# Kernel tuning notes

Hardware: AMD Instinct MI355X
Metric: run time of the kernel (lower is better)

Reference implementation:

```python
import jax, jax.numpy as jnp
import numpy as np

N_SECTORS = 10          # = 1.0 / slice_range with normalized slice indices in [0, 1)
SLICE_RANGE = 0.1
PAIRWISE_EPS = 1e-6     # torch.nn.functional.pairwise_distance default eps (added to the diff)


def setup_inputs() -> dict:
    key = jax.random.key(0)
    k1, k2, k3, k4 = jax.random.split(key, 4)
    source_embeddings = jax.random.normal(k1, (200000, 256), dtype=jnp.float32)
    source_sectors = jax.random.randint(k2, (200000,), 0, N_SECTORS, dtype=jnp.int32)
    target_embeddings = jax.random.normal(k3, (100000, 256), dtype=jnp.float32)
    target_slice_idx = jax.random.uniform(k4, (100000,), dtype=jnp.float32)
    return {
        "source_embeddings": source_embeddings,
        "source_sectors": source_sectors,
        "target_embeddings": target_embeddings,
        "target_slice_idx": target_slice_idx,
    }


def reference(source_embeddings, source_sectors, target_embeddings, target_slice_idx):
    # cluster_centers[i] = mean of source_embeddings where source_sectors == i
    sums = jax.ops.segment_sum(source_embeddings, source_sectors, num_segments=N_SECTORS)  # [S, D]
    counts = jax.ops.segment_sum(
        jnp.ones((source_embeddings.shape[0],), dtype=source_embeddings.dtype),
        source_sectors, num_segments=N_SECTORS)                                            # [S]
    cluster_centers = sums / counts[:, None]                                               # [S, D]

    # get_sectors_from_index: bucket normalized slice index into sectors of width slice_range
    target_sectors = jnp.clip(
        jnp.floor(target_slice_idx / SLICE_RANGE).astype(jnp.int32), 0, N_SECTORS - 1)     # [N]

    cc = cluster_centers[target_sectors]                                                   # [N, D] gather

    # F.pairwise_distance with p=2, eps=1e-6: ||x1 - x2 + eps||_2
    diff = target_embeddings - cc + PAIRWISE_EPS
    distances = jnp.sqrt(jnp.sum(diff * diff, axis=-1))                                    # [N]
    return distances.mean()
```

## Files before the change

kernel.cpp:

```cpp
#include <hip/hip_runtime.h>
#include <math.h>

#define D      256
#define NSEC   10
#define EPS    1e-6f
#define SLICE  0.1f

#define WS_SUMS 0
#define WS_CNT  (NSEC * D)
#define WS_DIST (NSEC * D + NSEC)
#define WS_ZERO_FLOATS (NSEC * D + NSEC + 1)

__global__ void k_zero(float* __restrict__ ws) {
    int i = blockIdx.x * blockDim.x + threadIdx.x;
    if (i < WS_ZERO_FLOATS) ws[i] = 0.f;
}

__global__ __launch_bounds__(256) void k_sums(const float* __restrict__ emb,
                                              const int* __restrict__ sec,
                                              float* __restrict__ ws, int nrows) {
    const int lane = threadIdx.x & 63;
    const int wid  = threadIdx.x >> 6;
    const int gw   = blockIdx.x * 4 + wid;
    const int nw   = gridDim.x * 4;

    float4 acc[NSEC];
    float  cnt[NSEC];
#pragma unroll
    for (int s = 0; s < NSEC; ++s) { acc[s] = make_float4(0.f, 0.f, 0.f, 0.f); cnt[s] = 0.f; }

    const float* ep = emb + (size_t)lane * 4;

    auto accum = [&](int sv, float4 v) {
        const int s = __builtin_amdgcn_readfirstlane(sv);
#pragma unroll
        for (int ss = 0; ss < NSEC; ++ss) {
            if (s == ss) {
                acc[ss].x += v.x; acc[ss].y += v.y; acc[ss].z += v.z; acc[ss].w += v.w;
                cnt[ss] += 1.f;
            }
        }
    };

    int r = gw;
    for (; r + 3 * nw < nrows; r += 4 * nw) {
        const int s0 = sec[r];
        const int s1 = sec[r + nw];
        const int s2 = sec[r + 2 * nw];
        const int s3 = sec[r + 3 * nw];
        const float4 v0 = *reinterpret_cast<const float4*>(ep + (size_t)r * D);
        const float4 v1 = *reinterpret_cast<const float4*>(ep + (size_t)(r + nw) * D);
        const float4 v2 = *reinterpret_cast<const float4*>(ep + (size_t)(r + 2 * nw) * D);
        const float4 v3 = *reinterpret_cast<const float4*>(ep + (size_t)(r + 3 * nw) * D);
        accum(s0, v0); accum(s1, v1); accum(s2, v2); accum(s3, v3);
    }
    for (; r < nrows; r += nw)
        accum(sec[r], *reinterpret_cast<const float4*>(ep + (size_t)r * D));

    __shared__ float lsum[NSEC * D];
    __shared__ float lcnt[NSEC];
    for (int i = threadIdx.x; i < NSEC * D; i += 256) lsum[i] = 0.f;
    if (threadIdx.x < NSEC) lcnt[threadIdx.x] = 0.f;
    __syncthreads();

    for (int w = 0; w < 4; ++w) {
        if (wid == w) {
#pragma unroll
            for (int ss = 0; ss < NSEC; ++ss) {
                float* p = &lsum[ss * D + lane * 4];
                p[0] += acc[ss].x; p[1] += acc[ss].y; p[2] += acc[ss].z; p[3] += acc[ss].w;
                if (lane == 0) lcnt[ss] += cnt[ss];
            }
        }
        __syncthreads();
    }

#pragma unroll
    for (int ss = 0; ss < NSEC; ++ss)
        atomicAdd(&ws[WS_SUMS + ss * D + threadIdx.x], lsum[ss * D + threadIdx.x]);
    if (threadIdx.x < NSEC)
        atomicAdd(&ws[WS_CNT + threadIdx.x], lcnt[threadIdx.x]);
}

__global__ __launch_bounds__(256) void k_dist(const float* __restrict__ temb,
                                              const float* __restrict__ tsl,
                                              float* __restrict__ ws, int nrows) {
    __shared__ float lc[NSEC * D];
    for (int i = threadIdx.x; i < NSEC * D; i += 256) {
        const int s = i >> 8;
        lc[i] = ws[WS_SUMS + i] / ws[WS_CNT + s];
    }
    __syncthreads();

    const int lane = threadIdx.x & 63;
    const int wid  = threadIdx.x >> 6;
    const int gw   = blockIdx.x * 4 + wid;
    const int nw   = gridDim.x * 4;

    const float* tp = temb + (size_t)lane * 4;

    auto rowdist = [&](float si, float4 v) -> float {
        int s = (int)floorf(si / SLICE);
        s = s < 0 ? 0 : (s > NSEC - 1 ? NSEC - 1 : s);
        const float4 c = *reinterpret_cast<const float4*>(&lc[s * D + lane * 4]);
        const float dx = v.x - c.x + EPS;
        const float dy = v.y - c.y + EPS;
        const float dz = v.z - c.z + EPS;
        const float dw = v.w - c.w + EPS;
        float loc = dx * dx + dy * dy + dz * dz + dw * dw;
#pragma unroll
        for (int off = 32; off >= 1; off >>= 1) loc += __shfl_xor(loc, off, 64);
        return loc;
    };

    float wacc = 0.f;
    int r = gw;
    for (; r + 3 * nw < nrows; r += 4 * nw) {
        const float t0 = tsl[r];
        const float t1 = tsl[r + nw];
        const float t2 = tsl[r + 2 * nw];
        const float t3 = tsl[r + 3 * nw];
        const float4 v0 = *reinterpret_cast<const float4*>(tp + (size_t)r * D);
        const float4 v1 = *reinterpret_cast<const float4*>(tp + (size_t)(r + nw) * D);
        const float4 v2 = *reinterpret_cast<const float4*>(tp + (size_t)(r + 2 * nw) * D);
        const float4 v3 = *reinterpret_cast<const float4*>(tp + (size_t)(r + 3 * nw) * D);
        float l0 = rowdist(t0, v0);
        float l1 = rowdist(t1, v1);
        float l2 = rowdist(t2, v2);
        float l3 = rowdist(t3, v3);
        if (lane == 0) wacc += sqrtf(l0) + sqrtf(l1) + sqrtf(l2) + sqrtf(l3);
    }
    for (; r < nrows; r += nw) {
        float l = rowdist(tsl[r], *reinterpret_cast<const float4*>(tp + (size_t)r * D));
        if (lane == 0) wacc += sqrtf(l);
    }

    __shared__ float wsum[4];
    if (lane == 0) wsum[wid] = wacc;
    __syncthreads();
    if (threadIdx.x == 0)
        atomicAdd(&ws[WS_DIST], wsum[0] + wsum[1] + wsum[2] + wsum[3]);
}

__global__ void k_final(const float* __restrict__ ws, float* __restrict__ out, float invN) {
    out[0] = ws[WS_DIST] * invN;
}

extern "C" void kernel_launch(void* const* d_in, const int* in_sizes, int n_in,
                              void* d_out, int out_size, void* d_ws, size_t ws_size,
                              hipStream_t stream) {
    const float* semb = (const float*)d_in[0];
    const int*   ssec = (const int*)d_in[1];
    const float* temb = (const float*)d_in[2];
    const float* tsl  = (const float*)d_in[3];
    float* ws  = (float*)d_ws;
    float* out = (float*)d_out;
    const int nS = in_sizes[1];
    const int nT = in_sizes[3];

    hipLaunchKernelGGL(k_zero, dim3((WS_ZERO_FLOATS + 255) / 256), dim3(256), 0, stream, ws);
    hipLaunchKernelGGL(k_sums, dim3(1024), dim3(256), 0, stream, semb, ssec, ws, nS);
    hipLaunchKernelGGL(k_dist, dim3(1024), dim3(256), 0, stream, temb, tsl, ws, nT);
    hipLaunchKernelGGL(k_final, dim3(1), dim3(1), 0, stream, ws, out, 1.0f / (float)nT);
}
```

Measured before the change: 112.9 us.

## Replace global atomics with per-block slabs and a dedicated center-reduction kernel

```diff
diff --git a/kernel.cpp b/kernel.cpp
--- a/kernel.cpp
+++ b/kernel.cpp
@@ -6,19 +6,19 @@
 #define EPS    1e-6f
 #define SLICE  0.1f
 
-#define WS_SUMS 0
-#define WS_CNT  (NSEC * D)
-#define WS_DIST (NSEC * D + NSEC)
-#define WS_ZERO_FLOATS (NSEC * D + NSEC + 1)
-
-__global__ void k_zero(float* __restrict__ ws) {
-    int i = blockIdx.x * blockDim.x + threadIdx.x;
-    if (i < WS_ZERO_FLOATS) ws[i] = 0.f;
-}
-
-__global__ __launch_bounds__(256) void k_sums(const float* __restrict__ emb,
-                                              const int* __restrict__ sec,
-                                              float* __restrict__ ws, int nrows) {
+#define NSUM_BLOCKS  1024
+#define NDIST_BLOCKS 1024
+#define SLAB_STRIDE  (NSEC * D + NSEC)
+
+#define WS_SLAB 0
+#define WS_CENT ((size_t)NSUM_BLOCKS * SLAB_STRIDE)
+#define WS_PART (WS_CENT + NSEC * D)
+#define WS_NEED ((WS_PART + NDIST_BLOCKS) * sizeof(float))
+
+
+__global__ __launch_bounds__(256) void k_sums_slab(const float* __restrict__ emb,
+                                                   const int* __restrict__ sec,
+                                                   float* __restrict__ ws, int nrows) {
     const int lane = threadIdx.x & 63;
     const int wid  = threadIdx.x >> 6;
     const int gw   = blockIdx.x * 4 + wid;
@@ -75,34 +75,58 @@
         __syncthreads();
     }
 
-#pragma unroll
-    for (int ss = 0; ss < NSEC; ++ss)
-        atomicAdd(&ws[WS_SUMS + ss * D + threadIdx.x], lsum[ss * D + threadIdx.x]);
-    if (threadIdx.x < NSEC)
-        atomicAdd(&ws[WS_CNT + threadIdx.x], lcnt[threadIdx.x]);
-}
-
-__global__ __launch_bounds__(256) void k_dist(const float* __restrict__ temb,
-                                              const float* __restrict__ tsl,
-                                              float* __restrict__ ws, int nrows) {
-    __shared__ float lc[NSEC * D];
-    for (int i = threadIdx.x; i < NSEC * D; i += 256) {
-        const int s = i >> 8;
-        lc[i] = ws[WS_SUMS + i] / ws[WS_CNT + s];
-    }
-    __syncthreads();
-
+    float* slab = ws + (size_t)blockIdx.x * SLAB_STRIDE;
+    for (int i = threadIdx.x; i < NSEC * D; i += 256) slab[i] = lsum[i];
+    if (threadIdx.x < NSEC) slab[NSEC * D + threadIdx.x] = lcnt[threadIdx.x];
+}
+
+__global__ __launch_bounds__(1024) void k_centers(float* __restrict__ ws) {
+    const int s = blockIdx.x;
+    const int t = threadIdx.x;
+    const int d  = t & 255;
+    const int ch = t >> 8;
+
+    __shared__ float red[1024];
+    __shared__ float part[4][256];
+
+    red[t] = ws[(size_t)t * SLAB_STRIDE + NSEC * D + s];
+    __syncthreads();
+    for (int off = 512; off >= 1; off >>= 1) {
+        if (t < off) red[t] += red[t + off];
+        __syncthreads();
+    }
+
+    float a0 = 0.f, a1 = 0.f, a2 = 0.f, a3 = 0.f;
+    const size_t base = (size_t)s * D + d;
+    for (int b = ch * 256; b < ch * 256 + 256; b += 4) {
+        a0 += ws[(size_t)b       * SLAB_STRIDE + base];
+        a1 += ws[(size_t)(b + 1) * SLAB_STRIDE + base];
+        a2 += ws[(size_t)(b + 2) * SLAB_STRIDE + base];
+        a3 += ws[(size_t)(b + 3) * SLAB_STRIDE + base];
+    }
+    part[ch][d] = a0 + a1 + a2 + a3;
+    __syncthreads();
+    if (t < 256)
+        ws[WS_CENT + (size_t)s * D + t] =
+            (part[0][t] + part[1][t] + part[2][t] + part[3][t]) / red[0];
+}
+
+__global__ __launch_bounds__(256) void k_dist_direct(const float* __restrict__ temb,
+                                                     const float* __restrict__ tsl,
+                                                     const float* __restrict__ cent,
+                                                     float* __restrict__ part, int nrows) {
     const int lane = threadIdx.x & 63;
     const int wid  = threadIdx.x >> 6;
     const int gw   = blockIdx.x * 4 + wid;
     const int nw   = gridDim.x * 4;
 
     const float* tp = temb + (size_t)lane * 4;
+    const float* cp = cent + (size_t)lane * 4;
 
     auto rowdist = [&](float si, float4 v) -> float {
         int s = (int)floorf(si / SLICE);
         s = s < 0 ? 0 : (s > NSEC - 1 ? NSEC - 1 : s);
-        const float4 c = *reinterpret_cast<const float4*>(&lc[s * D + lane * 4]);
+        const float4 c = *reinterpret_cast<const float4*>(cp + (size_t)s * D);
         const float dx = v.x - c.x + EPS;
         const float dy = v.y - c.y + EPS;
         const float dz = v.z - c.z + EPS;
@@ -139,11 +163,121 @@
     if (lane == 0) wsum[wid] = wacc;
     __syncthreads();
     if (threadIdx.x == 0)
-        atomicAdd(&ws[WS_DIST], wsum[0] + wsum[1] + wsum[2] + wsum[3]);
-}
-
-__global__ void k_final(const float* __restrict__ ws, float* __restrict__ out, float invN) {
-    out[0] = ws[WS_DIST] * invN;
+        part[blockIdx.x] = wsum[0] + wsum[1] + wsum[2] + wsum[3];
+}
+
+__global__ __launch_bounds__(1024) void k_final2(const float* __restrict__ part,
+                                                 float* __restrict__ out, float invN) {
+    float v = part[threadIdx.x];
+#pragma unroll
+    for (int off = 32; off >= 1; off >>= 1) v += __shfl_xor(v, off, 64);
+    __shared__ float s16[16];
+    if ((threadIdx.x & 63) == 0) s16[threadIdx.x >> 6] = v;
+    __syncthreads();
+    if (threadIdx.x == 0) {
+        float tot = 0.f;
+#pragma unroll
+        for (int k = 0; k < 16; ++k) tot += s16[k];
+        out[0] = tot * invN;
+    }
+}
+
+
+#define FB_SUMS 0
+#define FB_CNT  (NSEC * D)
+#define FB_PART (NSEC * D + NSEC)
+#define FB_ZERO (NSEC * D + NSEC)
+
+__global__ void fb_zero(float* __restrict__ ws) {
+    int i = blockIdx.x * blockDim.x + threadIdx.x;
+    if (i < FB_ZERO) ws[i] = 0.f;
+}
+
+__global__ __launch_bounds__(256) void fb_sums(const float* __restrict__ emb,
+                                               const int* __restrict__ sec,
+                                               float* __restrict__ ws, int nrows) {
+    const int lane = threadIdx.x & 63;
+    const int wid  = threadIdx.x >> 6;
+    const int gw   = blockIdx.x * 4 + wid;
+    const int nw   = gridDim.x * 4;
+    float4 acc[NSEC]; float cnt[NSEC];
+#pragma unroll
+    for (int s = 0; s < NSEC; ++s) { acc[s] = make_float4(0.f,0.f,0.f,0.f); cnt[s] = 0.f; }
+    const float* ep = emb + (size_t)lane * 4;
+    auto accum = [&](int sv, float4 v) {
+        const int s = __builtin_amdgcn_readfirstlane(sv);
+#pragma unroll
+        for (int ss = 0; ss < NSEC; ++ss)
+            if (s == ss) { acc[ss].x+=v.x; acc[ss].y+=v.y; acc[ss].z+=v.z; acc[ss].w+=v.w; cnt[ss]+=1.f; }
+    };
+    for (int r = gw; r < nrows; r += nw)
+        accum(sec[r], *reinterpret_cast<const float4*>(ep + (size_t)r * D));
+    __shared__ float lsum[NSEC * D]; __shared__ float lcnt[NSEC];
+    for (int i = threadIdx.x; i < NSEC * D; i += 256) lsum[i] = 0.f;
+    if (threadIdx.x < NSEC) lcnt[threadIdx.x] = 0.f;
+    __syncthreads();
+    for (int w = 0; w < 4; ++w) {
+        if (wid == w) {
+#pragma unroll
+            for (int ss = 0; ss < NSEC; ++ss) {
+                float* p = &lsum[ss * D + lane * 4];
+                p[0]+=acc[ss].x; p[1]+=acc[ss].y; p[2]+=acc[ss].z; p[3]+=acc[ss].w;
+                if (lane == 0) lcnt[ss] += cnt[ss];
+            }
+        }
+        __syncthreads();
+    }
+#pragma unroll
+    for (int ss = 0; ss < NSEC; ++ss)
+        atomicAdd(&ws[FB_SUMS + ss * D + threadIdx.x], lsum[ss * D + threadIdx.x]);
+    if (threadIdx.x < NSEC) atomicAdd(&ws[FB_CNT + threadIdx.x], lcnt[threadIdx.x]);
+}
+
+__global__ __launch_bounds__(256) void fb_dist(const float* __restrict__ temb,
+                                               const float* __restrict__ tsl,
+                                               float* __restrict__ ws, int nrows) {
+    __shared__ float lc[NSEC * D];
+    for (int i = threadIdx.x; i < NSEC * D; i += 256)
+        lc[i] = ws[FB_SUMS + i] / ws[FB_CNT + (i >> 8)];
+    __syncthreads();
+    const int lane = threadIdx.x & 63;
+    const int wid  = threadIdx.x >> 6;
+    const int gw   = blockIdx.x * 4 + wid;
+    const int nw   = gridDim.x * 4;
+    const float* tp = temb + (size_t)lane * 4;
+    float wacc = 0.f;
+    for (int r = gw; r < nrows; r += nw) {
+        const float si = tsl[r];
+        int s = (int)floorf(si / SLICE);
+        s = s < 0 ? 0 : (s > NSEC - 1 ? NSEC - 1 : s);
+        const float4 v = *reinterpret_cast<const float4*>(tp + (size_t)r * D);
+        const float4 c = *reinterpret_cast<const float4*>(&lc[s * D + lane * 4]);
+        const float dx = v.x-c.x+EPS, dy = v.y-c.y+EPS, dz = v.z-c.z+EPS, dw = v.w-c.w+EPS;
+        float loc = dx*dx + dy*dy + dz*dz + dw*dw;
+#pragma unroll
+        for (int off = 32; off >= 1; off >>= 1) loc += __shfl_xor(loc, off, 64);
+        if (lane == 0) wacc += sqrtf(loc);
+    }
+    __shared__ float wsum[4];
+    if (lane == 0) wsum[wid] = wacc;
+    __syncthreads();
+    if (threadIdx.x == 0) ws[FB_PART + blockIdx.x] = wsum[0]+wsum[1]+wsum[2]+wsum[3];
+}
+
+__global__ __launch_bounds__(1024) void fb_final(const float* __restrict__ ws,
+                                                 float* __restrict__ out, float invN) {
+    float v = ws[FB_PART + threadIdx.x];
+#pragma unroll
+    for (int off = 32; off >= 1; off >>= 1) v += __shfl_xor(v, off, 64);
+    __shared__ float s16[16];
+    if ((threadIdx.x & 63) == 0) s16[threadIdx.x >> 6] = v;
+    __syncthreads();
+    if (threadIdx.x == 0) {
+        float tot = 0.f;
+#pragma unroll
+        for (int k = 0; k < 16; ++k) tot += s16[k];
+        out[0] = tot * invN;
+    }
 }
 
 extern "C" void kernel_launch(void* const* d_in, const int* in_sizes, int n_in,
@@ -157,9 +291,20 @@
     float* out = (float*)d_out;
     const int nS = in_sizes[1];
     const int nT = in_sizes[3];
-
-    hipLaunchKernelGGL(k_zero, dim3((WS_ZERO_FLOATS + 255) / 256), dim3(256), 0, stream, ws);
-    hipLaunchKernelGGL(k_sums, dim3(1024), dim3(256), 0, stream, semb, ssec, ws, nS);
-    hipLaunchKernelGGL(k_dist, dim3(1024), dim3(256), 0, stream, temb, tsl, ws, nT);
-    hipLaunchKernelGGL(k_final, dim3(1), dim3(1), 0, stream, ws, out, 1.0f / (float)nT);
-}
+    const float invN = 1.0f / (float)nT;
+
+    if (ws_size >= WS_NEED) {
+        hipLaunchKernelGGL(k_sums_slab, dim3(NSUM_BLOCKS), dim3(256), 0, stream,
+                           semb, ssec, ws, nS);
+        hipLaunchKernelGGL(k_centers, dim3(NSEC), dim3(1024), 0, stream, ws);
+        hipLaunchKernelGGL(k_dist_direct, dim3(NDIST_BLOCKS), dim3(256), 0, stream,
+                           temb, tsl, ws + WS_CENT, ws + WS_PART, nT);
+        hipLaunchKernelGGL(k_final2, dim3(1), dim3(1024), 0, stream,
+                           ws + WS_PART, out, invN);
+    } else {
+        hipLaunchKernelGGL(fb_zero, dim3((FB_ZERO + 255) / 256), dim3(256), 0, stream, ws);
+        hipLaunchKernelGGL(fb_sums, dim3(1024), dim3(256), 0, stream, semb, ssec, ws, nS);
+        hipLaunchKernelGGL(fb_dist, dim3(1024), dim3(256), 0, stream, temb, tsl, ws, nT);
+        hipLaunchKernelGGL(fb_final, dim3(1), dim3(1024), 0, stream, ws, out, invN);
+    }
+}
```

Result: no change. 113.5 us (+0.6%).
